# Kernel tuning notes

Hardware: AMD Instinct MI355X
Metric: run time of the kernel (lower is better)

## Reference

```python
import jax, jax.numpy as jnp
import numpy as np

T = 48        # target_size
B = 128       # batch of sequences (vmapped version of the per-sequence module)
S = 512       # seq_len
START = 46    # start_index
END = 47      # end_index
MIN = 0.0001  # self.minimum


def setup_inputs() -> dict:
    key = jax.random.key(0)
    k1, k2 = jax.random.split(key)
    features = jax.random.normal(k1, (B, S, T), dtype=jnp.float32)
    # __init_transition__: uniform matrix with start column / end row zeroed,
    # then MIN placed at those zeroed positions.
    u = jax.random.uniform(k2, (T, T), dtype=jnp.float32)
    start_mask = 1.0 - jax.nn.one_hot(jnp.full((T,), START), T)          # zeros column START
    end_mask = 1.0 - jax.nn.one_hot(jnp.full((T,), END), T).T            # zeros row END
    value = (1.0 - start_mask * end_mask) * MIN                          # MIN where masked out
    transition = u * start_mask * end_mask + value
    return {"features": features, "transition": transition}


def reference(features, transition):
    # CRF forward (partition-function) score, faithful to forward_score(),
    # batched over B sequences. features: [B, S, T], transition: [T, T].
    fv0 = MIN * (1.0 - jax.nn.one_hot(START, T, dtype=jnp.float32))      # [T]
    fv0 = jnp.broadcast_to(fv0, (B, T))

    def step(fv, feat_t):
        # score[b, i, j] = fv[b, j] + transition[i, j] + feat_t[b, i]
        score = fv[:, None, :] + transition[None, :, :] + feat_t[:, :, None]  # [B, T, T]
        # Faithful replication of the source's log_sum_exp: the max subtracted
        # inside exp is the per-row max indexed by j (column position), while the
        # max added back is indexed by i.
        rowmax = jnp.max(score, axis=2)                                   # [B, T]
        new_fv = rowmax + jnp.log(jnp.sum(jnp.exp(score - rowmax[:, None, :]), axis=2))
        return new_fv, None

    feats_time_major = jnp.swapaxes(features, 0, 1)                       # [S, B, T]
    fv, _ = jax.lax.scan(step, fv0, feats_time_major)

    # Terminal transition to END, then a single-row logsumexp (standard here).
    sc = fv + transition[END][None, :]                                    # [B, T]
    m = jnp.max(sc, axis=1)                                               # [B]
    return m + jnp.log(jnp.sum(jnp.exp(sc - m[:, None]), axis=1))         # [B]
```

## Files before the change

kernel.cpp:

```cpp
#include <hip/hip_runtime.h>
#include <math.h>


#define TT 48
#define BB 128
#define SS 512
#define STARTI 46
#define ENDI 47
#define MINV 0.0001f
#define CHUNK 64
#define NCHUNK (SS / CHUNK)
#define LOG2E 1.44269504088896340736f
#define LN2   0.69314718055994530942f

#if __has_builtin(__builtin_amdgcn_exp2f)
#define EXP2F(x) __builtin_amdgcn_exp2f(x)
#else
#define EXP2F(x) exp2f(x)
#endif
#if __has_builtin(__builtin_amdgcn_logf)
#define LOG2F(x) __builtin_amdgcn_logf(x)
#else
#define LOG2F(x) log2f(x)
#endif

template <int CTRL>
__device__ __forceinline__ float qperm_f(float x) {
#if __has_builtin(__builtin_amdgcn_update_dpp)
    return __int_as_float(__builtin_amdgcn_update_dpp(
        0, __float_as_int(x), CTRL, 0xF, 0xF, true));
#elif __has_builtin(__builtin_amdgcn_mov_dpp)
    return __int_as_float(
        __builtin_amdgcn_mov_dpp(__float_as_int(x), CTRL, 0xF, 0xF, true));
#else
    return __shfl_xor(x, (CTRL == 0xB1) ? 1 : 2, 64);
#endif
}

__device__ __forceinline__ void sync_lds() {
    asm volatile("s_waitcnt lgkmcnt(0)" ::: "memory");
    __builtin_amdgcn_s_barrier();
    asm volatile("" ::: "memory");
}

__global__ __launch_bounds__(192, 1) void crf_forward_kernel(
    const float* __restrict__ feats,
    const float* __restrict__ trans,
    float* __restrict__ out)
{
    const int tid  = threadIdx.x;
    const int b    = blockIdx.x;
    const int i    = tid >> 2;
    const int jsub = tid & 3;
    const int j0   = jsub * 12;

    __shared__ __align__(16) float fv2[TT];
    __shared__ __align__(16) float hbuf[TT];
    __shared__ __align__(16) float featbuf[2][CHUNK * TT];

    float tr2[12], E[12];
#pragma unroll
    for (int q = 0; q < 3; ++q) {
        float4 v = *reinterpret_cast<const float4*>(trans + i * TT + j0 + 4 * q);
        tr2[4 * q + 0] = v.x * LOG2E; tr2[4 * q + 1] = v.y * LOG2E;
        tr2[4 * q + 2] = v.z * LOG2E; tr2[4 * q + 3] = v.w * LOG2E;
    }
#pragma unroll
    for (int q = 0; q < 12; ++q) E[q] = EXP2F(tr2[q]);

    const float* fb = feats + (size_t)b * SS * TT;

    float fv2i = (i == STARTI) ? 0.0f : (MINV * LOG2E);
    if (tid < TT) fv2[tid] = (tid == STARTI) ? 0.0f : (MINV * LOG2E);

#pragma unroll
    for (int k = 0; k < 4; ++k) {
        float4 v = *reinterpret_cast<const float4*>(fb + k * 768 + tid * 4);
        *reinterpret_cast<float4*>(&featbuf[0][k * 768 + tid * 4]) = v;
    }
    sync_lds();

    float feat2 = featbuf[0][i] * LOG2E;

    for (int c = 0; c < NCHUNK; ++c) {
        const int buf = c & 1;
        const bool hp = (c + 1 < NCHUNK);
        float4 pf[4];
        if (hp) {
            const float* src = fb + (c + 1) * (CHUNK * TT);
#pragma unroll
            for (int k = 0; k < 4; ++k)
                pf[k] = *reinterpret_cast<const float4*>(src + k * 768 + tid * 4);
        }
        const float* fbb = &featbuf[buf][0];
        const float* fbn = &featbuf[buf ^ 1][0];

#pragma unroll 2
        for (int sl = 0; sl < CHUNK; ++sl) {
            const float p2 = fv2i - feat2;
            const float featN = (sl + 1 < CHUNK) ? fbb[(sl + 1) * TT + i]
                                                 : fbn[i];

            float a[12];
#pragma unroll
            for (int q = 0; q < 3; ++q) {
                float4 v = *reinterpret_cast<const float4*>(&fv2[j0 + 4 * q]);
                a[4 * q + 0] = v.x + tr2[4 * q + 0];
                a[4 * q + 1] = v.y + tr2[4 * q + 1];
                a[4 * q + 2] = v.z + tr2[4 * q + 2];
                a[4 * q + 3] = v.w + tr2[4 * q + 3];
            }
            float m0 = fmaxf(fmaxf(a[0], a[1]),  a[2]);
            float m1 = fmaxf(fmaxf(a[3], a[4]),  a[5]);
            float m2 = fmaxf(fmaxf(a[6], a[7]),  a[8]);
            float m3 = fmaxf(fmaxf(a[9], a[10]), a[11]);
            float M2 = fmaxf(fmaxf(fmaxf(m0, m1), m2), m3);
            M2 = fmaxf(M2, qperm_f<0xB1>(M2));
            M2 = fmaxf(M2, qperm_f<0x4E>(M2));

            const float h = EXP2F(p2 - M2);
            if (jsub == 0) hbuf[i] = h;
            const float qv2 = M2 + 2.0f * feat2;
            sync_lds();

            float hv[12];
#pragma unroll
            for (int q = 0; q < 3; ++q) {
                float4 v = *reinterpret_cast<const float4*>(&hbuf[j0 + 4 * q]);
                hv[4 * q + 0] = v.x; hv[4 * q + 1] = v.y;
                hv[4 * q + 2] = v.z; hv[4 * q + 3] = v.w;
            }
            float d0 = E[0] * hv[0], d1 = E[1] * hv[1];
            float d2 = E[2] * hv[2], d3 = E[3] * hv[3];
            d0 = fmaf(E[4],  hv[4],  d0); d1 = fmaf(E[5],  hv[5],  d1);
            d2 = fmaf(E[6],  hv[6],  d2); d3 = fmaf(E[7],  hv[7],  d3);
            d0 = fmaf(E[8],  hv[8],  d0); d1 = fmaf(E[9],  hv[9],  d1);
            d2 = fmaf(E[10], hv[10], d2); d3 = fmaf(E[11], hv[11], d3);
            float dot = (d0 + d1) + (d2 + d3);
            dot += qperm_f<0xB1>(dot);
            dot += qperm_f<0x4E>(dot);

            const float nfv = qv2 + LOG2F(dot);
            fv2i = nfv;
            if (jsub == 0) fv2[i] = nfv;

            feat2 = featN * LOG2E;

            if (sl == 8 && hp) {
#pragma unroll
                for (int k = 0; k < 4; ++k)
                    *reinterpret_cast<float4*>(&featbuf[buf ^ 1][k * 768 + tid * 4]) = pf[k];
            }
            sync_lds();
        }
    }

    if (tid < 64) {
        const float* te = trans + ENDI * TT;
        float sc = (tid < TT) ? fmaf(fv2[tid], LN2, te[tid]) : -3.4e38f;
        float m = sc;
#pragma unroll
        for (int off = 32; off >= 1; off >>= 1)
            m = fmaxf(m, __shfl_xor(m, off));
        float e = (tid < TT) ? __expf(sc - m) : 0.0f;
#pragma unroll
        for (int off = 32; off >= 1; off >>= 1)
            e += __shfl_xor(e, off);
        if (tid == 0) out[b] = m + __logf(e);
    }
}

extern "C" void kernel_launch(void* const* d_in, const int* in_sizes, int n_in,
                              void* d_out, int out_size, void* d_ws, size_t ws_size,
                              hipStream_t stream) {
    (void)in_sizes; (void)n_in; (void)out_size; (void)d_ws; (void)ws_size;
    const float* feats = (const float*)d_in[0];
    const float* trans = (const float*)d_in[1];
    float* out = (float*)d_out;
    crf_forward_kernel<<<dim3(BB), dim3(192), 0, stream>>>(feats, trans, out);
}
```

Baseline: 230.4 us.

## Process four sequences per block to amortize barriers and use async LDS loads

```diff
diff --git a/kernel.cpp b/kernel.cpp
--- a/kernel.cpp
+++ b/kernel.cpp
@@ -8,8 +8,11 @@
 #define STARTI 46
 #define ENDI 47
 #define MINV 0.0001f
-#define CHUNK 64
+#define KSEQ 4
+#define NBLK (BB / KSEQ)
+#define CHUNK 32
 #define NCHUNK (SS / CHUNK)
+#define KPT 2
 #define LOG2E 1.44269504088896340736f
 #define LN2   0.69314718055994530942f
 
@@ -43,20 +46,32 @@
     asm volatile("" ::: "memory");
 }
 
+#if __has_builtin(__builtin_amdgcn_global_load_lds)
+#define HAVE_GLOAD 1
+__device__ __forceinline__ void gload16(const float* g, float* l) {
+    __builtin_amdgcn_global_load_lds(
+        (const __attribute__((address_space(1))) void*)g,
+        (__attribute__((address_space(3))) void*)l, 16, 0, 0);
+}
+#else
+#define HAVE_GLOAD 0
+#endif
+
 __global__ __launch_bounds__(192, 1) void crf_forward_kernel(
     const float* __restrict__ feats,
     const float* __restrict__ trans,
     float* __restrict__ out)
 {
     const int tid  = threadIdx.x;
-    const int b    = blockIdx.x;
     const int i    = tid >> 2;
     const int jsub = tid & 3;
     const int j0   = jsub * 12;
-
-    __shared__ __align__(16) float fv2[TT];
-    __shared__ __align__(16) float hbuf[TT];
-    __shared__ __align__(16) float featbuf[2][CHUNK * TT];
+    const int wv   = tid >> 6;
+    const int b0   = blockIdx.x * KSEQ;
+
+    __shared__ __align__(16) float fv2[KSEQ][TT];
+    __shared__ __align__(16) float hbuf[KSEQ][TT];
+    __shared__ __align__(16) float featbuf[KSEQ][2][CHUNK * TT];
 
     float tr2[12], E[12];
 #pragma unroll
@@ -68,105 +83,154 @@
 #pragma unroll
     for (int q = 0; q < 12; ++q) E[q] = EXP2F(tr2[q]);
 
-    const float* fb = feats + (size_t)b * SS * TT;
-
-    float fv2i = (i == STARTI) ? 0.0f : (MINV * LOG2E);
-    if (tid < TT) fv2[tid] = (tid == STARTI) ? 0.0f : (MINV * LOG2E);
-
-#pragma unroll
-    for (int k = 0; k < 4; ++k) {
-        float4 v = *reinterpret_cast<const float4*>(fb + k * 768 + tid * 4);
-        *reinterpret_cast<float4*>(&featbuf[0][k * 768 + tid * 4]) = v;
+    const float* fb[KSEQ];
+#pragma unroll
+    for (int s = 0; s < KSEQ; ++s)
+        fb[s] = feats + (size_t)(b0 + s) * SS * TT;
+
+#if HAVE_GLOAD
+#pragma unroll
+    for (int s = 0; s < KSEQ; ++s)
+#pragma unroll
+        for (int k = 0; k < KPT; ++k)
+            gload16(fb[s] + k * 768 + tid * 4,
+                    &featbuf[s][0][k * 768 + wv * 256]);
+    asm volatile("s_waitcnt vmcnt(0)" ::: "memory");
+#else
+#pragma unroll
+    for (int s = 0; s < KSEQ; ++s)
+#pragma unroll
+        for (int k = 0; k < KPT; ++k)
+            *reinterpret_cast<float4*>(&featbuf[s][0][k * 768 + tid * 4]) =
+                *reinterpret_cast<const float4*>(fb[s] + k * 768 + tid * 4);
+#endif
+
+    if (tid < TT) {
+#pragma unroll
+        for (int s = 0; s < KSEQ; ++s)
+            fv2[s][tid] = (tid == STARTI) ? 0.0f : (MINV * LOG2E);
     }
     sync_lds();
 
-    float feat2 = featbuf[0][i] * LOG2E;
+    float fv2i[KSEQ], feat2[KSEQ];
+#pragma unroll
+    for (int s = 0; s < KSEQ; ++s) {
+        fv2i[s]  = (i == STARTI) ? 0.0f : (MINV * LOG2E);
+        feat2[s] = featbuf[s][0][i] * LOG2E;
+    }
 
     for (int c = 0; c < NCHUNK; ++c) {
         const int buf = c & 1;
         const bool hp = (c + 1 < NCHUNK);
-        float4 pf[4];
-        if (hp) {
-            const float* src = fb + (c + 1) * (CHUNK * TT);
-#pragma unroll
-            for (int k = 0; k < 4; ++k)
-                pf[k] = *reinterpret_cast<const float4*>(src + k * 768 + tid * 4);
-        }
-        const float* fbb = &featbuf[buf][0];
-        const float* fbn = &featbuf[buf ^ 1][0];
-
-#pragma unroll 2
+
         for (int sl = 0; sl < CHUNK; ++sl) {
-            const float p2 = fv2i - feat2;
-            const float featN = (sl + 1 < CHUNK) ? fbb[(sl + 1) * TT + i]
-                                                 : fbn[i];
-
-            float a[12];
-#pragma unroll
-            for (int q = 0; q < 3; ++q) {
-                float4 v = *reinterpret_cast<const float4*>(&fv2[j0 + 4 * q]);
-                a[4 * q + 0] = v.x + tr2[4 * q + 0];
-                a[4 * q + 1] = v.y + tr2[4 * q + 1];
-                a[4 * q + 2] = v.z + tr2[4 * q + 2];
-                a[4 * q + 3] = v.w + tr2[4 * q + 3];
-            }
-            float m0 = fmaxf(fmaxf(a[0], a[1]),  a[2]);
-            float m1 = fmaxf(fmaxf(a[3], a[4]),  a[5]);
-            float m2 = fmaxf(fmaxf(a[6], a[7]),  a[8]);
-            float m3 = fmaxf(fmaxf(a[9], a[10]), a[11]);
-            float M2 = fmaxf(fmaxf(fmaxf(m0, m1), m2), m3);
-            M2 = fmaxf(M2, qperm_f<0xB1>(M2));
-            M2 = fmaxf(M2, qperm_f<0x4E>(M2));
-
-            const float h = EXP2F(p2 - M2);
-            if (jsub == 0) hbuf[i] = h;
-            const float qv2 = M2 + 2.0f * feat2;
+            if (sl == 0 && hp) {
+#if HAVE_GLOAD
+#pragma unroll
+                for (int s = 0; s < KSEQ; ++s)
+#pragma unroll
+                    for (int k = 0; k < KPT; ++k)
+                        gload16(fb[s] + (c + 1) * (CHUNK * TT) + k * 768 + tid * 4,
+                                &featbuf[s][buf ^ 1][k * 768 + wv * 256]);
+#else
+#pragma unroll
+                for (int s = 0; s < KSEQ; ++s)
+#pragma unroll
+                    for (int k = 0; k < KPT; ++k)
+                        *reinterpret_cast<float4*>(&featbuf[s][buf ^ 1][k * 768 + tid * 4]) =
+                            *reinterpret_cast<const float4*>(
+                                fb[s] + (c + 1) * (CHUNK * TT) + k * 768 + tid * 4);
+#endif
+            }
+
+            float4 va[KSEQ][3];
+#pragma unroll
+            for (int s = 0; s < KSEQ; ++s)
+#pragma unroll
+                for (int q = 0; q < 3; ++q)
+                    va[s][q] = *reinterpret_cast<const float4*>(&fv2[s][j0 + 4 * q]);
+            float featN[KSEQ];
+#pragma unroll
+            for (int s = 0; s < KSEQ; ++s)
+                featN[s] = (sl + 1 < CHUNK) ? featbuf[s][buf][(sl + 1) * TT + i]
+                                            : featbuf[s][buf ^ 1][i];
+
+            float hs[KSEQ], qv2[KSEQ];
+#pragma unroll
+            for (int s = 0; s < KSEQ; ++s) {
+                float a[12];
+                a[0]  = va[s][0].x + tr2[0];  a[1]  = va[s][0].y + tr2[1];
+                a[2]  = va[s][0].z + tr2[2];  a[3]  = va[s][0].w + tr2[3];
+                a[4]  = va[s][1].x + tr2[4];  a[5]  = va[s][1].y + tr2[5];
+                a[6]  = va[s][1].z + tr2[6];  a[7]  = va[s][1].w + tr2[7];
+                a[8]  = va[s][2].x + tr2[8];  a[9]  = va[s][2].y + tr2[9];
+                a[10] = va[s][2].z + tr2[10]; a[11] = va[s][2].w + tr2[11];
+                float m0 = fmaxf(fmaxf(a[0], a[1]),  a[2]);
+                float m1 = fmaxf(fmaxf(a[3], a[4]),  a[5]);
+                float m2 = fmaxf(fmaxf(a[6], a[7]),  a[8]);
+                float m3 = fmaxf(fmaxf(a[9], a[10]), a[11]);
+                float M2 = fmaxf(fmaxf(fmaxf(m0, m1), m2), m3);
+                M2 = fmaxf(M2, qperm_f<0xB1>(M2));
+                M2 = fmaxf(M2, qperm_f<0x4E>(M2));
+                hs[s]  = EXP2F((fv2i[s] - feat2[s]) - M2);
+                qv2[s] = M2 + 2.0f * feat2[s];
+            }
+            if (jsub == 0) {
+#pragma unroll
+                for (int s = 0; s < KSEQ; ++s) hbuf[s][i] = hs[s];
+            }
             sync_lds();
 
-            float hv[12];
-#pragma unroll
-            for (int q = 0; q < 3; ++q) {
-                float4 v = *reinterpret_cast<const float4*>(&hbuf[j0 + 4 * q]);
-                hv[4 * q + 0] = v.x; hv[4 * q + 1] = v.y;
-                hv[4 * q + 2] = v.z; hv[4 * q + 3] = v.w;
-            }
-            float d0 = E[0] * hv[0], d1 = E[1] * hv[1];
-            float d2 = E[2] * hv[2], d3 = E[3] * hv[3];
-            d0 = fmaf(E[4],  hv[4],  d0); d1 = fmaf(E[5],  hv[5],  d1);
-            d2 = fmaf(E[6],  hv[6],  d2); d3 = fmaf(E[7],  hv[7],  d3);
-            d0 = fmaf(E[8],  hv[8],  d0); d1 = fmaf(E[9],  hv[9],  d1);
-            d2 = fmaf(E[10], hv[10], d2); d3 = fmaf(E[11], hv[11], d3);
-            float dot = (d0 + d1) + (d2 + d3);
-            dot += qperm_f<0xB1>(dot);
-            dot += qperm_f<0x4E>(dot);
-
-            const float nfv = qv2 + LOG2F(dot);
-            fv2i = nfv;
-            if (jsub == 0) fv2[i] = nfv;
-
-            feat2 = featN * LOG2E;
-
-            if (sl == 8 && hp) {
-#pragma unroll
-                for (int k = 0; k < 4; ++k)
-                    *reinterpret_cast<float4*>(&featbuf[buf ^ 1][k * 768 + tid * 4]) = pf[k];
-            }
+            float4 vh[KSEQ][3];
+#pragma unroll
+            for (int s = 0; s < KSEQ; ++s)
+#pragma unroll
+                for (int q = 0; q < 3; ++q)
+                    vh[s][q] = *reinterpret_cast<const float4*>(&hbuf[s][j0 + 4 * q]);
+
+            float nfv[KSEQ];
+#pragma unroll
+            for (int s = 0; s < KSEQ; ++s) {
+                float d0 = E[0] * vh[s][0].x, d1 = E[1] * vh[s][0].y;
+                float d2 = E[2] * vh[s][0].z, d3 = E[3] * vh[s][0].w;
+                d0 = fmaf(E[4],  vh[s][1].x, d0); d1 = fmaf(E[5],  vh[s][1].y, d1);
+                d2 = fmaf(E[6],  vh[s][1].z, d2); d3 = fmaf(E[7],  vh[s][1].w, d3);
+                d0 = fmaf(E[8],  vh[s][2].x, d0); d1 = fmaf(E[9],  vh[s][2].y, d1);
+                d2 = fmaf(E[10], vh[s][2].z, d2); d3 = fmaf(E[11], vh[s][2].w, d3);
+                float dot = (d0 + d1) + (d2 + d3);
+                dot += qperm_f<0xB1>(dot);
+                dot += qperm_f<0x4E>(dot);
+                nfv[s]   = qv2[s] + LOG2F(dot);
+                fv2i[s]  = nfv[s];
+                feat2[s] = featN[s] * LOG2E;
+            }
+            if (jsub == 0) {
+#pragma unroll
+                for (int s = 0; s < KSEQ; ++s) fv2[s][i] = nfv[s];
+            }
+#if HAVE_GLOAD
+            if (sl == CHUNK - 2)
+                asm volatile("s_waitcnt vmcnt(0)" ::: "memory");
+#endif
             sync_lds();
         }
     }
 
     if (tid < 64) {
         const float* te = trans + ENDI * TT;
-        float sc = (tid < TT) ? fmaf(fv2[tid], LN2, te[tid]) : -3.4e38f;
-        float m = sc;
-#pragma unroll
-        for (int off = 32; off >= 1; off >>= 1)
-            m = fmaxf(m, __shfl_xor(m, off));
-        float e = (tid < TT) ? __expf(sc - m) : 0.0f;
-#pragma unroll
-        for (int off = 32; off >= 1; off >>= 1)
-            e += __shfl_xor(e, off);
-        if (tid == 0) out[b] = m + __logf(e);
+#pragma unroll
+        for (int s = 0; s < KSEQ; ++s) {
+            float sc = (tid < TT) ? fmaf(fv2[s][tid], LN2, te[tid]) : -3.4e38f;
+            float m = sc;
+#pragma unroll
+            for (int off = 32; off >= 1; off >>= 1)
+                m = fmaxf(m, __shfl_xor(m, off));
+            float e = (tid < TT) ? __expf(sc - m) : 0.0f;
+#pragma unroll
+            for (int off = 32; off >= 1; off >>= 1)
+                e += __shfl_xor(e, off);
+            if (tid == 0) out[b0 + s] = m + __logf(e);
+        }
     }
 }
 
@@ -177,5 +241,5 @@
     const float* feats = (const float*)d_in[0];
     const float* trans = (const float*)d_in[1];
     float* out = (float*)d_out;
-    crf_forward_kernel<<<dim3(BB), dim3(192), 0, stream>>>(feats, trans, out);
-}
+    crf_forward_kernel<<<dim3(NBLK), dim3(192), 0, stream>>>(feats, trans, out);
+}
```

Result: slower. 489.0 us (+112.2%).

## Shrink CRF block to one wavefront, dropping barriers and using async LDS loads

Applied to the files above, without the earlier changes.

```diff
diff --git a/kernel.cpp b/kernel.cpp
--- a/kernel.cpp
+++ b/kernel.cpp
@@ -8,8 +8,9 @@
 #define STARTI 46
 #define ENDI 47
 #define MINV 0.0001f
-#define CHUNK 64
+#define CHUNK 32
 #define NCHUNK (SS / CHUNK)
+#define GPT 6
 #define LOG2E 1.44269504088896340736f
 #define LN2   0.69314718055994530942f
 
@@ -37,136 +38,172 @@
 #endif
 }
 
-__device__ __forceinline__ void sync_lds() {
-    asm volatile("s_waitcnt lgkmcnt(0)" ::: "memory");
-    __builtin_amdgcn_s_barrier();
-    asm volatile("" ::: "memory");
-}
-
-__global__ __launch_bounds__(192, 1) void crf_forward_kernel(
+#if __has_builtin(__builtin_amdgcn_global_load_lds)
+#define HAVE_GLOAD 1
+__device__ __forceinline__ void gload16(const float* g, float* l) {
+    __builtin_amdgcn_global_load_lds(
+        (const __attribute__((address_space(1))) void*)g,
+        (__attribute__((address_space(3))) void*)l, 16, 0, 0);
+}
+#else
+#define HAVE_GLOAD 0
+#endif
+
+__global__ __launch_bounds__(64, 1) void crf_forward_kernel(
     const float* __restrict__ feats,
     const float* __restrict__ trans,
     float* __restrict__ out)
 {
-    const int tid  = threadIdx.x;
+    const int lane = threadIdx.x;
+    const int i16  = lane >> 2;
+    const int jsub = lane & 3;
+    const int j0   = jsub * 12;
     const int b    = blockIdx.x;
-    const int i    = tid >> 2;
-    const int jsub = tid & 3;
-    const int j0   = jsub * 12;
-
-    __shared__ __align__(16) float fv2[TT];
-    __shared__ __align__(16) float hbuf[TT];
+
+    __shared__ __align__(16) float fvb[TT];
+    __shared__ __align__(16) float hb[TT];
     __shared__ __align__(16) float featbuf[2][CHUNK * TT];
 
-    float tr2[12], E[12];
-#pragma unroll
-    for (int q = 0; q < 3; ++q) {
-        float4 v = *reinterpret_cast<const float4*>(trans + i * TT + j0 + 4 * q);
-        tr2[4 * q + 0] = v.x * LOG2E; tr2[4 * q + 1] = v.y * LOG2E;
-        tr2[4 * q + 2] = v.z * LOG2E; tr2[4 * q + 3] = v.w * LOG2E;
+    float tr2[3][12], E[3][12];
+#pragma unroll
+    for (int r = 0; r < 3; ++r) {
+#pragma unroll
+        for (int q = 0; q < 3; ++q) {
+            float4 v = *reinterpret_cast<const float4*>(
+                trans + (i16 + 16 * r) * TT + j0 + 4 * q);
+            tr2[r][4 * q + 0] = v.x * LOG2E; tr2[r][4 * q + 1] = v.y * LOG2E;
+            tr2[r][4 * q + 2] = v.z * LOG2E; tr2[r][4 * q + 3] = v.w * LOG2E;
+        }
+#pragma unroll
+        for (int q = 0; q < 12; ++q) E[r][q] = EXP2F(tr2[r][q]);
     }
-#pragma unroll
-    for (int q = 0; q < 12; ++q) E[q] = EXP2F(tr2[q]);
 
     const float* fb = feats + (size_t)b * SS * TT;
 
-    float fv2i = (i == STARTI) ? 0.0f : (MINV * LOG2E);
-    if (tid < TT) fv2[tid] = (tid == STARTI) ? 0.0f : (MINV * LOG2E);
-
-#pragma unroll
-    for (int k = 0; k < 4; ++k) {
-        float4 v = *reinterpret_cast<const float4*>(fb + k * 768 + tid * 4);
-        *reinterpret_cast<float4*>(&featbuf[0][k * 768 + tid * 4]) = v;
-    }
-    sync_lds();
-
-    float feat2 = featbuf[0][i] * LOG2E;
+#if HAVE_GLOAD
+#pragma unroll
+    for (int k = 0; k < GPT; ++k)
+        gload16(fb + k * 256 + lane * 4, &featbuf[0][k * 256]);
+#else
+#pragma unroll
+    for (int k = 0; k < GPT; ++k)
+        *reinterpret_cast<float4*>(&featbuf[0][k * 256 + lane * 4]) =
+            *reinterpret_cast<const float4*>(fb + k * 256 + lane * 4);
+#endif
+
+    if (lane < TT) fvb[lane] = (lane == STARTI) ? 0.0f : (MINV * LOG2E);
+    float fvi[3];
+#pragma unroll
+    for (int r = 0; r < 3; ++r)
+        fvi[r] = ((i16 + 16 * r) == STARTI) ? 0.0f : (MINV * LOG2E);
+
+#if HAVE_GLOAD
+    asm volatile("s_waitcnt vmcnt(0)" ::: "memory");
+#endif
 
     for (int c = 0; c < NCHUNK; ++c) {
         const int buf = c & 1;
         const bool hp = (c + 1 < NCHUNK);
-        float4 pf[4];
         if (hp) {
-            const float* src = fb + (c + 1) * (CHUNK * TT);
-#pragma unroll
-            for (int k = 0; k < 4; ++k)
-                pf[k] = *reinterpret_cast<const float4*>(src + k * 768 + tid * 4);
-        }
-        const float* fbb = &featbuf[buf][0];
-        const float* fbn = &featbuf[buf ^ 1][0];
-
-#pragma unroll 2
+#if HAVE_GLOAD
+#pragma unroll
+            for (int k = 0; k < GPT; ++k)
+                gload16(fb + (c + 1) * (CHUNK * TT) + k * 256 + lane * 4,
+                        &featbuf[buf ^ 1][k * 256]);
+#else
+#pragma unroll
+            for (int k = 0; k < GPT; ++k)
+                *reinterpret_cast<float4*>(&featbuf[buf ^ 1][k * 256 + lane * 4]) =
+                    *reinterpret_cast<const float4*>(
+                        fb + (c + 1) * (CHUNK * TT) + k * 256 + lane * 4);
+#endif
+        }
+
         for (int sl = 0; sl < CHUNK; ++sl) {
-            const float p2 = fv2i - feat2;
-            const float featN = (sl + 1 < CHUNK) ? fbb[(sl + 1) * TT + i]
-                                                 : fbn[i];
-
-            float a[12];
-#pragma unroll
-            for (int q = 0; q < 3; ++q) {
-                float4 v = *reinterpret_cast<const float4*>(&fv2[j0 + 4 * q]);
-                a[4 * q + 0] = v.x + tr2[4 * q + 0];
-                a[4 * q + 1] = v.y + tr2[4 * q + 1];
-                a[4 * q + 2] = v.z + tr2[4 * q + 2];
-                a[4 * q + 3] = v.w + tr2[4 * q + 3];
-            }
-            float m0 = fmaxf(fmaxf(a[0], a[1]),  a[2]);
-            float m1 = fmaxf(fmaxf(a[3], a[4]),  a[5]);
-            float m2 = fmaxf(fmaxf(a[6], a[7]),  a[8]);
-            float m3 = fmaxf(fmaxf(a[9], a[10]), a[11]);
-            float M2 = fmaxf(fmaxf(fmaxf(m0, m1), m2), m3);
-            M2 = fmaxf(M2, qperm_f<0xB1>(M2));
-            M2 = fmaxf(M2, qperm_f<0x4E>(M2));
-
-            const float h = EXP2F(p2 - M2);
-            if (jsub == 0) hbuf[i] = h;
-            const float qv2 = M2 + 2.0f * feat2;
-            sync_lds();
-
-            float hv[12];
-#pragma unroll
-            for (int q = 0; q < 3; ++q) {
-                float4 v = *reinterpret_cast<const float4*>(&hbuf[j0 + 4 * q]);
-                hv[4 * q + 0] = v.x; hv[4 * q + 1] = v.y;
-                hv[4 * q + 2] = v.z; hv[4 * q + 3] = v.w;
-            }
-            float d0 = E[0] * hv[0], d1 = E[1] * hv[1];
-            float d2 = E[2] * hv[2], d3 = E[3] * hv[3];
-            d0 = fmaf(E[4],  hv[4],  d0); d1 = fmaf(E[5],  hv[5],  d1);
-            d2 = fmaf(E[6],  hv[6],  d2); d3 = fmaf(E[7],  hv[7],  d3);
-            d0 = fmaf(E[8],  hv[8],  d0); d1 = fmaf(E[9],  hv[9],  d1);
-            d2 = fmaf(E[10], hv[10], d2); d3 = fmaf(E[11], hv[11], d3);
-            float dot = (d0 + d1) + (d2 + d3);
-            dot += qperm_f<0xB1>(dot);
-            dot += qperm_f<0x4E>(dot);
-
-            const float nfv = qv2 + LOG2F(dot);
-            fv2i = nfv;
-            if (jsub == 0) fv2[i] = nfv;
-
-            feat2 = featN * LOG2E;
-
-            if (sl == 8 && hp) {
-#pragma unroll
-                for (int k = 0; k < 4; ++k)
-                    *reinterpret_cast<float4*>(&featbuf[buf ^ 1][k * 768 + tid * 4]) = pf[k];
-            }
-            sync_lds();
+            float feat2[3];
+#pragma unroll
+            for (int r = 0; r < 3; ++r)
+                feat2[r] = featbuf[buf][sl * TT + i16 + 16 * r] * LOG2E;
+
+            float4 v0 = *reinterpret_cast<const float4*>(&fvb[j0]);
+            float4 v1 = *reinterpret_cast<const float4*>(&fvb[j0 + 4]);
+            float4 v2 = *reinterpret_cast<const float4*>(&fvb[j0 + 8]);
+            float fvs[12] = {v0.x, v0.y, v0.z, v0.w, v1.x, v1.y,
+                             v1.z, v1.w, v2.x, v2.y, v2.z, v2.w};
+
+            float hs[3], qv2[3];
+#pragma unroll
+            for (int r = 0; r < 3; ++r) {
+                float a[12];
+#pragma unroll
+                for (int q = 0; q < 12; ++q) a[q] = fvs[q] + tr2[r][q];
+                float m0 = fmaxf(fmaxf(a[0], a[1]),  a[2]);
+                float m1 = fmaxf(fmaxf(a[3], a[4]),  a[5]);
+                float m2 = fmaxf(fmaxf(a[6], a[7]),  a[8]);
+                float m3 = fmaxf(fmaxf(a[9], a[10]), a[11]);
+                float M2 = fmaxf(fmaxf(fmaxf(m0, m1), m2), m3);
+                M2 = fmaxf(M2, qperm_f<0xB1>(M2));
+                M2 = fmaxf(M2, qperm_f<0x4E>(M2));
+                hs[r]  = EXP2F((fvi[r] - feat2[r]) - M2);
+                qv2[r] = M2 + 2.0f * feat2[r];
+            }
+            if (jsub == 0) {
+                hb[i16]      = hs[0];
+                hb[i16 + 16] = hs[1];
+                hb[i16 + 32] = hs[2];
+            }
+            float4 h0 = *reinterpret_cast<const float4*>(&hb[j0]);
+            float4 h1 = *reinterpret_cast<const float4*>(&hb[j0 + 4]);
+            float4 h2 = *reinterpret_cast<const float4*>(&hb[j0 + 8]);
+            float hv[12] = {h0.x, h0.y, h0.z, h0.w, h1.x, h1.y,
+                            h1.z, h1.w, h2.x, h2.y, h2.z, h2.w};
+
+            float nfv[3];
+#pragma unroll
+            for (int r = 0; r < 3; ++r) {
+                float d0 = E[r][0] * hv[0], d1 = E[r][1] * hv[1];
+                float d2 = E[r][2] * hv[2], d3 = E[r][3] * hv[3];
+                d0 = fmaf(E[r][4],  hv[4],  d0); d1 = fmaf(E[r][5],  hv[5],  d1);
+                d2 = fmaf(E[r][6],  hv[6],  d2); d3 = fmaf(E[r][7],  hv[7],  d3);
+                d0 = fmaf(E[r][8],  hv[8],  d0); d1 = fmaf(E[r][9],  hv[9],  d1);
+                d2 = fmaf(E[r][10], hv[10], d2); d3 = fmaf(E[r][11], hv[11], d3);
+                float dot = (d0 + d1) + (d2 + d3);
+                dot += qperm_f<0xB1>(dot);
+                dot += qperm_f<0x4E>(dot);
+                nfv[r] = qv2[r] + LOG2F(dot);
+                fvi[r] = nfv[r];
+            }
+            if (jsub == 0) {
+                fvb[i16]      = nfv[0];
+                fvb[i16 + 16] = nfv[1];
+                fvb[i16 + 32] = nfv[2];
+            }
+#if HAVE_GLOAD
+            if (sl == CHUNK - 2 && hp)
+                asm volatile("s_waitcnt vmcnt(0)" ::: "memory");
+#endif
         }
     }
 
-    if (tid < 64) {
+    {
         const float* te = trans + ENDI * TT;
-        float sc = (tid < TT) ? fmaf(fv2[tid], LN2, te[tid]) : -3.4e38f;
-        float m = sc;
-#pragma unroll
-        for (int off = 32; off >= 1; off >>= 1)
-            m = fmaxf(m, __shfl_xor(m, off));
-        float e = (tid < TT) ? __expf(sc - m) : 0.0f;
-#pragma unroll
-        for (int off = 32; off >= 1; off >>= 1)
-            e += __shfl_xor(e, off);
-        if (tid == 0) out[b] = m + __logf(e);
+        float sc[TT];
+#pragma unroll
+        for (int q = 0; q < 12; ++q) {
+            float4 fv4 = *reinterpret_cast<const float4*>(&fvb[4 * q]);
+            float4 te4 = *reinterpret_cast<const float4*>(te + 4 * q);
+            sc[4 * q + 0] = fmaf(fv4.x, LN2, te4.x);
+            sc[4 * q + 1] = fmaf(fv4.y, LN2, te4.y);
+            sc[4 * q + 2] = fmaf(fv4.z, LN2, te4.z);
+            sc[4 * q + 3] = fmaf(fv4.w, LN2, te4.w);
+        }
+        float m = sc[0];
+#pragma unroll
+        for (int j = 1; j < TT; ++j) m = fmaxf(m, sc[j]);
+        float s = 0.0f;
+#pragma unroll
+        for (int j = 0; j < TT; ++j) s += __expf(sc[j] - m);
+        if (lane == 0) out[b] = m + __logf(s);
     }
 }
 
@@ -177,5 +214,5 @@
     const float* feats = (const float*)d_in[0];
     const float* trans = (const float*)d_in[1];
     float* out = (float*)d_out;
-    crf_forward_kernel<<<dim3(BB), dim3(192), 0, stream>>>(feats, trans, out);
-}
+    crf_forward_kernel<<<dim3(BB), dim3(64), 0, stream>>>(feats, trans, out);
+}
```

After: 258.2 us. +12.1%, slower.
